# Kernel optimization log

Measured on AMD Instinct MI355X. Metric: run time of the kernel, lower is better.

## Reference

```python
import jax, jax.numpy as jnp
import numpy as np
import math

B, S, D, H = 2, 2048, 1024, 16
DH = D // H  # head_size = 64


def setup_inputs() -> dict:
    key = jax.random.key(0)
    ks = jax.random.split(key, 11)
    s = 0.02
    return {
        "queries": jax.random.normal(ks[0], (B, S, D), jnp.float32),
        "keys": jax.random.normal(ks[1], (B, S, D), jnp.float32),
        "values": jax.random.normal(ks[2], (B, S, D), jnp.float32),
        # nn.Linear weights: y = x @ W.T + b, W has shape (out, in)
        "W_Q": jax.random.normal(ks[3], (D, D), jnp.float32) * s,
        "b_Q": jax.random.normal(ks[4], (D,), jnp.float32) * s,
        "W_K": jax.random.normal(ks[5], (D, D), jnp.float32) * s,
        "b_K": jax.random.normal(ks[6], (D,), jnp.float32) * s,
        "W_V": jax.random.normal(ks[7], (D, D), jnp.float32) * s,
        "b_V": jax.random.normal(ks[8], (D,), jnp.float32) * s,
        "W_O": jax.random.normal(ks[9], (D, D), jnp.float32) * s,
        "b_O": jax.random.normal(ks[10], (D,), jnp.float32) * s,
    }


def _split_heads(x):
    # (B, S, H*DH) -> (B, H, S, DH); torch.chunk+stack == reshape+transpose
    b, s, _ = x.shape
    return x.reshape(b, s, H, DH).transpose(0, 2, 1, 3)


def reference(queries, keys, values, W_Q, b_Q, W_K, b_K, W_V, b_V, W_O, b_O):
    q = _split_heads(queries @ W_Q.T + b_Q)  # (B,H,S,DH)
    k = _split_heads(keys @ W_K.T + b_K)
    v = _split_heads(values @ W_V.T + b_V)

    scale = 1.0 / math.sqrt(DH)
    scores = jnp.einsum("bhqd,bhkd->bhqk", q, k) * scale  # (B,H,S,S)
    causal = jnp.tril(jnp.ones((S, S), dtype=bool))  # allow j <= i (causal)
    scores = jnp.where(causal, scores, -jnp.inf)
    weights = jax.nn.softmax(scores, axis=-1)

    attended = jnp.einsum("bhqk,bhkd->bhqd", weights, v)  # (B,H,S,DH)
    merged = attended.transpose(0, 2, 1, 3).reshape(B, S, D)  # merge_heads
    return merged @ W_O.T + b_O
```

## Files before the change

### kernel.cpp

```cpp
#include <hip/hip_runtime.h>


typedef __bf16 bf16x8 __attribute__((ext_vector_type(8)));
typedef __bf16 bf16x4 __attribute__((ext_vector_type(4)));
typedef float  f32x4  __attribute__((ext_vector_type(4)));
typedef int    i32x2  __attribute__((ext_vector_type(2)));
typedef int    i32x4  __attribute__((ext_vector_type(4)));

#define B_  2
#define S_  2048
#define D_  1024
#define H_  16
#define DH_ 64

#define NEG_ 1.0e30f
#define M2_  5.77078016f
#define QSCALE_ 0.18033688f

#if __has_builtin(__builtin_amdgcn_exp2f)
#define EXP2(x) __builtin_amdgcn_exp2f(x)
#else
#define EXP2(x) __builtin_exp2f(x)
#endif

__device__ __forceinline__ void load_lds16(const __bf16* g, __bf16* lds_base) {
    __builtin_amdgcn_global_load_lds(
        (const __attribute__((address_space(1))) void*)g,
        (__attribute__((address_space(3))) void*)lds_base,
        16, 0, 0);
}

__device__ __forceinline__ int pack_bf16(float lo, float hi) {
    union { int u; __bf16 h[2]; } r;
    r.h[0] = (__bf16)lo; r.h[1] = (__bf16)hi;
    return r.u;
}

__device__ __forceinline__ void p32swap(int& a, int& b, int lane) {
#if __has_builtin(__builtin_amdgcn_permlane32_swap)
    i32x2 r = __builtin_amdgcn_permlane32_swap(a, b, false, false);
    a = r[0]; b = r[1];
#else
    const int addr = ((lane ^ 32) & 63) << 2;
    int ax = __builtin_amdgcn_ds_bpermute(addr, a);
    int bx = __builtin_amdgcn_ds_bpermute(addr, b);
    int na = (lane < 32) ? a : bx;
    int nb = (lane < 32) ? ax : b;
    a = na; b = nb;
#endif
}
__device__ __forceinline__ void p16swap(int& a, int& b, int lane) {
#if __has_builtin(__builtin_amdgcn_permlane16_swap)
    i32x2 r = __builtin_amdgcn_permlane16_swap(a, b, false, false);
    a = r[0]; b = r[1];
#else
    int as = __builtin_amdgcn_ds_swizzle(a, 0x401F);
    int bs = __builtin_amdgcn_ds_swizzle(b, 0x401F);
    const bool odd = (lane >> 4) & 1;
    int na = odd ? bs : a;
    int nb = odd ? b : as;
    a = na; b = nb;
#endif
}

__device__ __forceinline__ bf16x8 cvt8(const float* __restrict__ p) {
    const float4 a = *(const float4*)p;
    const float4 b = *(const float4*)(p + 4);
    bf16x8 r;
    r[0] = (__bf16)a.x; r[1] = (__bf16)a.y; r[2] = (__bf16)a.z; r[3] = (__bf16)a.w;
    r[4] = (__bf16)b.x; r[5] = (__bf16)b.y; r[6] = (__bf16)b.z; r[7] = (__bf16)b.w;
    return r;
}

__global__ void cvt_kernel(const float* __restrict__ q, const float* __restrict__ k,
                           const float* __restrict__ v,
                           const float* __restrict__ wq, const float* __restrict__ wk,
                           const float* __restrict__ wv, const float* __restrict__ wo,
                           __bf16* __restrict__ qb, __bf16* __restrict__ kb,
                           __bf16* __restrict__ vb,
                           __bf16* __restrict__ wqb, __bf16* __restrict__ wkb,
                           __bf16* __restrict__ wvb, __bf16* __restrict__ wob) {
    const int z = blockIdx.z;
    const float* src; __bf16* dst; size_t n;
    switch (z) {
        case 0: src = q;  dst = qb;  n = (size_t)B_ * S_ * D_; break;
        case 1: src = k;  dst = kb;  n = (size_t)B_ * S_ * D_; break;
        case 2: src = v;  dst = vb;  n = (size_t)B_ * S_ * D_; break;
        case 3: src = wq; dst = wqb; n = (size_t)D_ * D_; break;
        case 4: src = wk; dst = wkb; n = (size_t)D_ * D_; break;
        case 5: src = wv; dst = wvb; n = (size_t)D_ * D_; break;
        default: src = wo; dst = wob; n = (size_t)D_ * D_; break;
    }
    const size_t i = ((size_t)blockIdx.x * 256 + threadIdx.x) * 8;
    if (i >= n) return;
    *(bf16x8*)(dst + i) = cvt8(src + i);
}

__device__ __forceinline__ void gemm128_bf(const __bf16* __restrict__ X,
                                           const __bf16* __restrict__ W,
                                           int m0, int n0, int K,
                                           __bf16* As, __bf16* Bs,
                                           f32x4 acc[4][4]) {
    const int tid  = threadIdx.x;
    const int wave = tid >> 6, lane = tid & 63;
    const int row  = lane & 15, quad = lane >> 4;
    const int wm   = wave >> 1, wn = wave & 1;
    const int arow = lane >> 2;
    const int acol = (lane & 3) * 8;

    const f32x4 fzero = {0.f, 0.f, 0.f, 0.f};
#pragma unroll
    for (int mt = 0; mt < 4; ++mt)
#pragma unroll
        for (int nt = 0; nt < 4; ++nt) acc[mt][nt] = fzero;

    auto stage = [&](int buf, int k0) {
#pragma unroll
        for (int c = 0; c < 2; ++c) {
            const int j = wave * 2 + c;
            load_lds16(X + (size_t)(m0 + j * 16 + arow) * K + k0 + acol,
                       As + buf * 4096 + j * 512);
            load_lds16(W + (size_t)(n0 + j * 16 + arow) * K + k0 + acol,
                       Bs + buf * 4096 + j * 512);
        }
    };

    stage(0, 0);
    int cur = 0;
    for (int k0 = 0; k0 < K; k0 += 32) {
        __syncthreads();
        if (k0 + 32 < K) stage(cur ^ 1, k0 + 32);
        const __bf16* Ab = As + cur * 4096;
        const __bf16* Bb = Bs + cur * 4096;
        bf16x8 af[4], bfv[4];
#pragma unroll
        for (int t = 0; t < 4; ++t) {
            af[t]  = *(const bf16x8*)(Ab + (wm * 64 + t * 16 + row) * 32 + quad * 8);
            bfv[t] = *(const bf16x8*)(Bb + (wn * 64 + t * 16 + row) * 32 + quad * 8);
        }
        __builtin_amdgcn_s_setprio(1);
#pragma unroll
        for (int mt = 0; mt < 4; ++mt)
#pragma unroll
            for (int nt = 0; nt < 4; ++nt)
                acc[mt][nt] = __builtin_amdgcn_mfma_f32_16x16x32_bf16(
                    af[mt], bfv[nt], acc[mt][nt], 0, 0, 0);
        __builtin_amdgcn_s_setprio(0);
        cur ^= 1;
    }
}

__global__ void qkv_kernel(const __bf16* __restrict__ qb, const __bf16* __restrict__ kb,
                           const __bf16* __restrict__ vb,
                           const __bf16* __restrict__ wqb, const __bf16* __restrict__ wkb,
                           const __bf16* __restrict__ wvb,
                           const float* __restrict__ bq, const float* __restrict__ bk,
                           const float* __restrict__ bv,
                           __bf16* __restrict__ q_ws, __bf16* __restrict__ k_ws,
                           __bf16* __restrict__ v_ws) {
    __shared__ __align__(16) __bf16 SMEM[16384];
    __bf16* As = SMEM;
    __bf16* Bs = SMEM + 8192;

    const int mode = blockIdx.z;
    const __bf16* X    = mode == 0 ? qb : mode == 1 ? kb : vb;
    const __bf16* W    = mode == 0 ? wqb : mode == 1 ? wkb : wvb;
    const float*  bias = mode == 0 ? bq : mode == 1 ? bk : bv;
    const int m0 = blockIdx.y * 128, n0 = blockIdx.x * 128;

    f32x4 acc[4][4];
    gemm128_bf(X, W, m0, n0, D_, As, Bs, acc);

    const int tid = threadIdx.x;
    const int wave = tid >> 6, lane = tid & 63;
    const int row = lane & 15, quad = lane >> 4;
    const int wm = wave >> 1, wn = wave & 1;

    if (mode == 2) {
        __syncthreads();
        __bf16* T = SMEM;
#pragma unroll
        for (int nt = 0; nt < 4; ++nt) {
            const int nloc = wn * 64 + nt * 16 + row;
            const float bf = bias[n0 + nloc];
#pragma unroll
            for (int mt = 0; mt < 4; ++mt)
#pragma unroll
                for (int r2 = 0; r2 < 4; ++r2) {
                    const int mloc = wm * 64 + mt * 16 + quad * 4 + r2;
                    T[nloc * 128 + ((((mloc >> 3) ^ (nloc & 15)) << 3) | (mloc & 7))] =
                        (__bf16)(acc[mt][nt][r2] + bf);
                }
        }
        __syncthreads();
#pragma unroll
        for (int p = 0; p < 8; ++p) {
            const int nloc = p * 16 + (tid >> 4);
            const int k = tid & 15;
            bf16x8 vv = *(const bf16x8*)(T + nloc * 128 + ((k ^ (nloc & 15)) << 3));
            const int n = n0 + nloc;
            const int h = n >> 6, dh = n & 63;
            const int m = m0 + k * 8;
            const int bb = m >> 11, s = m & (S_ - 1);
            *(bf16x8*)(v_ws + (((size_t)bb * H_ + h) * DH_ + dh) * S_ + s) = vv;
        }
        return;
    }

#pragma unroll
    for (int nt = 0; nt < 4; ++nt) {
        const int n  = n0 + wn * 64 + nt * 16 + row;
        const float bf = bias[n];
        const int h = n >> 6, dh = n & 63;
#pragma unroll
        for (int mt = 0; mt < 4; ++mt) {
#pragma unroll
            for (int r2 = 0; r2 < 4; ++r2) {
                const int m = m0 + wm * 64 + mt * 16 + quad * 4 + r2;
                const int bb = m >> 11, s = m & (S_ - 1);
                const float val = acc[mt][nt][r2] + bf;
                if (mode == 0)
                    q_ws[(((size_t)bb * H_ + h) * S_ + s) * DH_ + dh] = (__bf16)(val * QSCALE_);
                else
                    k_ws[(((size_t)bb * H_ + h) * S_ + s) * DH_ + dh] = (__bf16)val;
            }
        }
    }
}

__global__ __launch_bounds__(256, 4)
void attn_kernel(const __bf16* __restrict__ q_ws, const __bf16* __restrict__ k_ws,
                 const __bf16* __restrict__ v_ws, __bf16* __restrict__ att) {
    __shared__ __align__(16) __bf16 Ks[2 * 64 * 64];
    __shared__ __align__(16) __bf16 Vs[2 * 64 * 64];

    const int id = blockIdx.x;
    const int bh = (id & 7) * 4 + ((id >> 3) & 3);
    const int u = id >> 5, ua = u >> 3, uj = u & 7;
    const int qt = ua * 8 + ((ua & 1) ? (7 - uj) : uj);
    const int tid = threadIdx.x, wave = tid >> 6, lane = tid & 63;
    const int row = lane & 15, quad = lane >> 4;

    const __bf16* Qg = q_ws + ((size_t)bh * S_ + qt * 64 + wave * 16) * DH_;
    const __bf16* Kg = k_ws + (size_t)bh * S_ * DH_;
    const __bf16* Vg = v_ws + (size_t)bh * DH_ * S_;

    bf16x8 qf[2];
#pragma unroll
    for (int ks = 0; ks < 2; ++ks)
        qf[ks] = *(const bf16x8*)(Qg + row * DH_ + ks * 32 + quad * 8);

    bf16x8 onesf;
#pragma unroll
    for (int i = 0; i < 8; ++i) onesf[i] = (__bf16)1.0f;

    const f32x4 fzero = {0.f, 0.f, 0.f, 0.f};
    f32x4 oacc[4];
    f32x4 lacc = fzero;
#pragma unroll
    for (int dt = 0; dt < 4; ++dt) oacc[dt] = fzero;

    const int srow = lane >> 3;
    const int scol = ((lane & 7) ^ srow) * 8;
    const int nkv = qt + 1;

    auto stage = [&](int buf, int kv) {
        __bf16* Kd = Ks + buf * 4096;
        __bf16* Vd = Vs + buf * 4096;
#pragma unroll
        for (int c = 0; c < 2; ++c) {
            const int ck = wave * 2 + c;
            load_lds16(Kg + (size_t)(kv * 64 + ck * 8 + srow) * DH_ + scol, Kd + ck * 512);
            load_lds16(Vg + (size_t)(ck * 8 + srow) * S_ + kv * 64 + scol, Vd + ck * 512);
        }
    };

    stage(0, 0);
    int cur = 0;
    for (int kv = 0; kv < nkv; ++kv) {
        __syncthreads();
        if (kv + 1 < nkv) stage(cur ^ 1, kv + 1);
        const bool diag = (kv == nkv - 1);
        const __bf16* Kb = Ks + cur * 4096;
        const __bf16* Vb = Vs + cur * 4096;
        const int swz = (row & 7) << 3;

#pragma unroll
        for (int kc = 0; kc < 2; ++kc) {
            f32x4 s[2];
            s[0] = fzero; s[1] = fzero;
            __builtin_amdgcn_s_setprio(1);
#pragma unroll
            for (int jn = 0; jn < 2; ++jn) {
                const int nt = kc * 2 + jn;
                const int kb = (nt * 16 + row) * 64 + quad * 8;
                bf16x8 kf0 = *(const bf16x8*)(Kb + (kb ^ swz));
                bf16x8 kf1 = *(const bf16x8*)(Kb + ((kb + 32) ^ swz));
                s[jn] = __builtin_amdgcn_mfma_f32_16x16x32_bf16(kf0, qf[0], s[jn], 0, 0, 0);
                s[jn] = __builtin_amdgcn_mfma_f32_16x16x32_bf16(kf1, qf[1], s[jn], 0, 0, 0);
            }
            __builtin_amdgcn_s_setprio(0);

            if (diag) {
                const int rloc = wave * 16 + row;
#pragma unroll
                for (int jn = 0; jn < 2; ++jn)
#pragma unroll
                    for (int r = 0; r < 4; ++r) {
                        const int cloc = kc * 32 + jn * 16 + quad * 4 + r;
                        if (cloc > rloc) s[jn][r] = -NEG_;
                    }
            }

            float p0[4], p1[4];
#pragma unroll
            for (int r = 0; r < 4; ++r) {
                p0[r] = EXP2(s[0][r] - M2_);
                p1[r] = EXP2(s[1][r] - M2_);
            }
            int a0 = pack_bf16(p0[0], p0[1]), a1 = pack_bf16(p0[2], p0[3]);
            int b0 = pack_bf16(p1[0], p1[1]), b1 = pack_bf16(p1[2], p1[3]);
            p32swap(a0, b0, lane); p16swap(a0, b0, lane);
            p32swap(a1, b1, lane); p16swap(a1, b1, lane);
            union { i32x4 i; bf16x8 v; } pu;
            pu.i = (i32x4){a0, a1, b0, b1};
            const bf16x8 pf = pu.v;

            __builtin_amdgcn_s_setprio(1);
#pragma unroll
            for (int dt = 0; dt < 4; ++dt) {
                const int vb = (dt * 16 + row) * 64 + kc * 32 + quad * 8;
                bf16x8 vf = *(const bf16x8*)(Vb + (vb ^ swz));
                oacc[dt] = __builtin_amdgcn_mfma_f32_16x16x32_bf16(vf, pf, oacc[dt], 0, 0, 0);
            }
            lacc = __builtin_amdgcn_mfma_f32_16x16x32_bf16(onesf, pf, lacc, 0, 0, 0);
            __builtin_amdgcn_s_setprio(0);
        }
        cur ^= 1;
    }

    const int b = bh >> 4, h = bh & 15;
    const float inv = 1.f / lacc[0];
    const int srow2 = qt * 64 + wave * 16 + row;
    __bf16* obase = att + ((size_t)b * S_ + srow2) * D_ + h * DH_;
#pragma unroll
    for (int dt = 0; dt < 4; ++dt) {
        bf16x4 o;
#pragma unroll
        for (int r = 0; r < 4; ++r) o[r] = (__bf16)(oacc[dt][r] * inv);
        *(bf16x4*)(obase + dt * 16 + quad * 4) = o;
    }
}

__global__ void oproj_kernel(const __bf16* __restrict__ attn, const __bf16* __restrict__ wob,
                             const float* __restrict__ bo, float* __restrict__ out) {
    __shared__ __align__(16) __bf16 SMEM[16384];
    __bf16* As = SMEM;
    __bf16* Bs = SMEM + 8192;
    const int m0 = blockIdx.y * 128, n0 = blockIdx.x * 128;

    f32x4 acc[4][4];
    gemm128_bf(attn, wob, m0, n0, D_, As, Bs, acc);

    const int tid = threadIdx.x;
    const int wave = tid >> 6, lane = tid & 63;
    const int row = lane & 15, quad = lane >> 4;
    const int wm = wave >> 1, wn = wave & 1;

#pragma unroll
    for (int nt = 0; nt < 4; ++nt) {
        const int n = n0 + wn * 64 + nt * 16 + row;
        const float bf = bo[n];
#pragma unroll
        for (int mt = 0; mt < 4; ++mt) {
#pragma unroll
            for (int r = 0; r < 4; ++r) {
                const int m = m0 + wm * 64 + mt * 16 + quad * 4 + r;
                out[(size_t)m * D_ + n] = acc[mt][nt][r] + bf;
            }
        }
    }
}

extern "C" void kernel_launch(void* const* d_in, const int* in_sizes, int n_in,
                              void* d_out, int out_size, void* d_ws, size_t ws_size,
                              hipStream_t stream) {
    const float* q_in = (const float*)d_in[0];
    const float* k_in = (const float*)d_in[1];
    const float* v_in = (const float*)d_in[2];
    const float* wq   = (const float*)d_in[3];
    const float* bq   = (const float*)d_in[4];
    const float* wk   = (const float*)d_in[5];
    const float* bk   = (const float*)d_in[6];
    const float* wv   = (const float*)d_in[7];
    const float* bv   = (const float*)d_in[8];
    const float* wo   = (const float*)d_in[9];
    const float* bo   = (const float*)d_in[10];

    char* ws = (char*)d_ws;
    const size_t MB = 1024 * 1024;
    __bf16* qb   = (__bf16*)(ws);
    __bf16* kb   = (__bf16*)(ws + 8 * MB);
    __bf16* vb   = (__bf16*)(ws + 16 * MB);
    __bf16* wqb  = (__bf16*)(ws + 24 * MB);
    __bf16* wkb  = (__bf16*)(ws + 26 * MB);
    __bf16* wvb  = (__bf16*)(ws + 28 * MB);
    __bf16* wob  = (__bf16*)(ws + 30 * MB);
    __bf16* q_ws = (__bf16*)(ws + 32 * MB);
    __bf16* k_ws = (__bf16*)(ws + 40 * MB);
    __bf16* v_ws = (__bf16*)(ws + 48 * MB);
    __bf16* attb = qb;
    float*  out  = (float*)d_out;

    cvt_kernel<<<dim3(2048, 1, 7), 256, 0, stream>>>(
        q_in, k_in, v_in, wq, wk, wv, wo, qb, kb, vb, wqb, wkb, wvb, wob);
    qkv_kernel<<<dim3(D_ / 128, (B_ * S_) / 128, 3), 256, 0, stream>>>(
        qb, kb, vb, wqb, wkb, wvb, bq, bk, bv, q_ws, k_ws, v_ws);
    attn_kernel<<<dim3(32 * 32), 256, 0, stream>>>(q_ws, k_ws, v_ws, attb);
    oproj_kernel<<<dim3(D_ / 128, (B_ * S_) / 128), 256, 0, stream>>>(attb, wob, bo, out);
}
```

Measured before the change: 209.2 us.

## Pair complementary causal query tiles per attention block to share K/V loads

Each attention block now handles two query tiles, j and 31-j, so every block does the same amount of causal work. K/V tiles staged in LDS, and the K fragments read from them, are reused by both tiles, which halves the grid to 512 blocks. Launch bounds drop to 2 blocks per SM to leave room for the doubled accumulators and Q fragments. In exchange, register pressure rises, occupancy may fall, and the branches on act1 add control flow.

```diff
diff --git a/kernel.cpp b/kernel.cpp
--- a/kernel.cpp
+++ b/kernel.cpp
@@ -228,7 +228,7 @@
     }
 }
 
-__global__ __launch_bounds__(256, 4)
+__global__ __launch_bounds__(256, 2)
 void attn_kernel(const __bf16* __restrict__ q_ws, const __bf16* __restrict__ k_ws,
                  const __bf16* __restrict__ v_ws, __bf16* __restrict__ att) {
     __shared__ __align__(16) __bf16 Ks[2 * 64 * 64];
@@ -236,33 +236,42 @@
 
     const int id = blockIdx.x;
     const int bh = (id & 7) * 4 + ((id >> 3) & 3);
-    const int u = id >> 5, ua = u >> 3, uj = u & 7;
-    const int qt = ua * 8 + ((ua & 1) ? (7 - uj) : uj);
+    const int u = (id >> 5) & 7;
+    const int j = (id >> 8) ? (15 - u) : u;
+    const int qt0 = 31 - j, qt1 = j;
     const int tid = threadIdx.x, wave = tid >> 6, lane = tid & 63;
     const int row = lane & 15, quad = lane >> 4;
 
-    const __bf16* Qg = q_ws + ((size_t)bh * S_ + qt * 64 + wave * 16) * DH_;
     const __bf16* Kg = k_ws + (size_t)bh * S_ * DH_;
     const __bf16* Vg = v_ws + (size_t)bh * DH_ * S_;
 
-    bf16x8 qf[2];
-#pragma unroll
-    for (int ks = 0; ks < 2; ++ks)
-        qf[ks] = *(const bf16x8*)(Qg + row * DH_ + ks * 32 + quad * 8);
+    bf16x8 qf[2][2];
+#pragma unroll
+    for (int st = 0; st < 2; ++st) {
+        const int qts = st ? qt1 : qt0;
+        const __bf16* Qg = q_ws + ((size_t)bh * S_ + qts * 64 + wave * 16) * DH_;
+#pragma unroll
+        for (int ks = 0; ks < 2; ++ks)
+            qf[st][ks] = *(const bf16x8*)(Qg + row * DH_ + ks * 32 + quad * 8);
+    }
 
     bf16x8 onesf;
 #pragma unroll
     for (int i = 0; i < 8; ++i) onesf[i] = (__bf16)1.0f;
 
     const f32x4 fzero = {0.f, 0.f, 0.f, 0.f};
-    f32x4 oacc[4];
-    f32x4 lacc = fzero;
-#pragma unroll
-    for (int dt = 0; dt < 4; ++dt) oacc[dt] = fzero;
+    f32x4 oacc[2][4];
+    f32x4 lacc[2];
+#pragma unroll
+    for (int st = 0; st < 2; ++st) {
+        lacc[st] = fzero;
+#pragma unroll
+        for (int dt = 0; dt < 4; ++dt) oacc[st][dt] = fzero;
+    }
 
     const int srow = lane >> 3;
     const int scol = ((lane & 7) ^ srow) * 8;
-    const int nkv = qt + 1;
+    const int nkv = qt0 + 1;
 
     auto stage = [&](int buf, int kv) {
         __bf16* Kd = Ks + buf * 4096;
@@ -280,75 +289,113 @@
     for (int kv = 0; kv < nkv; ++kv) {
         __syncthreads();
         if (kv + 1 < nkv) stage(cur ^ 1, kv + 1);
-        const bool diag = (kv == nkv - 1);
         const __bf16* Kb = Ks + cur * 4096;
         const __bf16* Vb = Vs + cur * 4096;
+        const bool act1 = (kv <= qt1);
         const int swz = (row & 7) << 3;
 
 #pragma unroll
         for (int kc = 0; kc < 2; ++kc) {
-            f32x4 s[2];
-            s[0] = fzero; s[1] = fzero;
+            bf16x8 kf[2][2];
+#pragma unroll
+            for (int jn = 0; jn < 2; ++jn) {
+                const int kb = ((kc * 2 + jn) * 16 + row) * 64 + quad * 8;
+                kf[jn][0] = *(const bf16x8*)(Kb + (kb ^ swz));
+                kf[jn][1] = *(const bf16x8*)(Kb + ((kb + 32) ^ swz));
+            }
+            f32x4 s[2][2];
             __builtin_amdgcn_s_setprio(1);
 #pragma unroll
             for (int jn = 0; jn < 2; ++jn) {
-                const int nt = kc * 2 + jn;
-                const int kb = (nt * 16 + row) * 64 + quad * 8;
-                bf16x8 kf0 = *(const bf16x8*)(Kb + (kb ^ swz));
-                bf16x8 kf1 = *(const bf16x8*)(Kb + ((kb + 32) ^ swz));
-                s[jn] = __builtin_amdgcn_mfma_f32_16x16x32_bf16(kf0, qf[0], s[jn], 0, 0, 0);
-                s[jn] = __builtin_amdgcn_mfma_f32_16x16x32_bf16(kf1, qf[1], s[jn], 0, 0, 0);
+                s[0][jn] = fzero;
+                s[0][jn] = __builtin_amdgcn_mfma_f32_16x16x32_bf16(kf[jn][0], qf[0][0], s[0][jn], 0, 0, 0);
+                s[0][jn] = __builtin_amdgcn_mfma_f32_16x16x32_bf16(kf[jn][1], qf[0][1], s[0][jn], 0, 0, 0);
+            }
+            if (act1) {
+#pragma unroll
+                for (int jn = 0; jn < 2; ++jn) {
+                    s[1][jn] = fzero;
+                    s[1][jn] = __builtin_amdgcn_mfma_f32_16x16x32_bf16(kf[jn][0], qf[1][0], s[1][jn], 0, 0, 0);
+                    s[1][jn] = __builtin_amdgcn_mfma_f32_16x16x32_bf16(kf[jn][1], qf[1][1], s[1][jn], 0, 0, 0);
+                }
             }
             __builtin_amdgcn_s_setprio(0);
 
-            if (diag) {
-                const int rloc = wave * 16 + row;
+            const int rloc = wave * 16 + row;
+            if (kv == qt0) {
 #pragma unroll
                 for (int jn = 0; jn < 2; ++jn)
 #pragma unroll
                     for (int r = 0; r < 4; ++r) {
                         const int cloc = kc * 32 + jn * 16 + quad * 4 + r;
-                        if (cloc > rloc) s[jn][r] = -NEG_;
+                        if (cloc > rloc) s[0][jn][r] = -NEG_;
                     }
             }
-
-            float p0[4], p1[4];
-#pragma unroll
-            for (int r = 0; r < 4; ++r) {
-                p0[r] = EXP2(s[0][r] - M2_);
-                p1[r] = EXP2(s[1][r] - M2_);
-            }
-            int a0 = pack_bf16(p0[0], p0[1]), a1 = pack_bf16(p0[2], p0[3]);
-            int b0 = pack_bf16(p1[0], p1[1]), b1 = pack_bf16(p1[2], p1[3]);
-            p32swap(a0, b0, lane); p16swap(a0, b0, lane);
-            p32swap(a1, b1, lane); p16swap(a1, b1, lane);
-            union { i32x4 i; bf16x8 v; } pu;
-            pu.i = (i32x4){a0, a1, b0, b1};
-            const bf16x8 pf = pu.v;
+            if (act1 && kv == qt1) {
+#pragma unroll
+                for (int jn = 0; jn < 2; ++jn)
+#pragma unroll
+                    for (int r = 0; r < 4; ++r) {
+                        const int cloc = kc * 32 + jn * 16 + quad * 4 + r;
+                        if (cloc > rloc) s[1][jn][r] = -NEG_;
+                    }
+            }
+
+            bf16x8 pf[2];
+            {
+                int a0 = pack_bf16(EXP2(s[0][0][0] - M2_), EXP2(s[0][0][1] - M2_));
+                int a1 = pack_bf16(EXP2(s[0][0][2] - M2_), EXP2(s[0][0][3] - M2_));
+                int b0 = pack_bf16(EXP2(s[0][1][0] - M2_), EXP2(s[0][1][1] - M2_));
+                int b1 = pack_bf16(EXP2(s[0][1][2] - M2_), EXP2(s[0][1][3] - M2_));
+                p32swap(a0, b0, lane); p16swap(a0, b0, lane);
+                p32swap(a1, b1, lane); p16swap(a1, b1, lane);
+                union { i32x4 i; bf16x8 v; } pu;
+                pu.i = (i32x4){a0, a1, b0, b1};
+                pf[0] = pu.v;
+            }
+            if (act1) {
+                int a0 = pack_bf16(EXP2(s[1][0][0] - M2_), EXP2(s[1][0][1] - M2_));
+                int a1 = pack_bf16(EXP2(s[1][0][2] - M2_), EXP2(s[1][0][3] - M2_));
+                int b0 = pack_bf16(EXP2(s[1][1][0] - M2_), EXP2(s[1][1][1] - M2_));
+                int b1 = pack_bf16(EXP2(s[1][1][2] - M2_), EXP2(s[1][1][3] - M2_));
+                p32swap(a0, b0, lane); p16swap(a0, b0, lane);
+                p32swap(a1, b1, lane); p16swap(a1, b1, lane);
+                union { i32x4 i; bf16x8 v; } pu;
+                pu.i = (i32x4){a0, a1, b0, b1};
+                pf[1] = pu.v;
+            }
 
             __builtin_amdgcn_s_setprio(1);
 #pragma unroll
             for (int dt = 0; dt < 4; ++dt) {
                 const int vb = (dt * 16 + row) * 64 + kc * 32 + quad * 8;
                 bf16x8 vf = *(const bf16x8*)(Vb + (vb ^ swz));
-                oacc[dt] = __builtin_amdgcn_mfma_f32_16x16x32_bf16(vf, pf, oacc[dt], 0, 0, 0);
-            }
-            lacc = __builtin_amdgcn_mfma_f32_16x16x32_bf16(onesf, pf, lacc, 0, 0, 0);
+                oacc[0][dt] = __builtin_amdgcn_mfma_f32_16x16x32_bf16(vf, pf[0], oacc[0][dt], 0, 0, 0);
+                if (act1)
+                    oacc[1][dt] = __builtin_amdgcn_mfma_f32_16x16x32_bf16(vf, pf[1], oacc[1][dt], 0, 0, 0);
+            }
+            lacc[0] = __builtin_amdgcn_mfma_f32_16x16x32_bf16(onesf, pf[0], lacc[0], 0, 0, 0);
+            if (act1)
+                lacc[1] = __builtin_amdgcn_mfma_f32_16x16x32_bf16(onesf, pf[1], lacc[1], 0, 0, 0);
             __builtin_amdgcn_s_setprio(0);
         }
         cur ^= 1;
     }
 
     const int b = bh >> 4, h = bh & 15;
-    const float inv = 1.f / lacc[0];
-    const int srow2 = qt * 64 + wave * 16 + row;
-    __bf16* obase = att + ((size_t)b * S_ + srow2) * D_ + h * DH_;
-#pragma unroll
-    for (int dt = 0; dt < 4; ++dt) {
-        bf16x4 o;
-#pragma unroll
-        for (int r = 0; r < 4; ++r) o[r] = (__bf16)(oacc[dt][r] * inv);
-        *(bf16x4*)(obase + dt * 16 + quad * 4) = o;
+#pragma unroll
+    for (int st = 0; st < 2; ++st) {
+        const int qts = st ? qt1 : qt0;
+        const float inv = 1.f / lacc[st][0];
+        const int srow2 = qts * 64 + wave * 16 + row;
+        __bf16* obase = att + ((size_t)b * S_ + srow2) * D_ + h * DH_;
+#pragma unroll
+        for (int dt = 0; dt < 4; ++dt) {
+            bf16x4 o;
+#pragma unroll
+            for (int r = 0; r < 4; ++r) o[r] = (__bf16)(oacc[st][dt][r] * inv);
+            *(bf16x4*)(obase + dt * 16 + quad * 4) = o;
+        }
     }
 }
 
@@ -416,6 +463,6 @@
         q_in, k_in, v_in, wq, wk, wv, wo, qb, kb, vb, wqb, wkb, wvb, wob);
     qkv_kernel<<<dim3(D_ / 128, (B_ * S_) / 128, 3), 256, 0, stream>>>(
         qb, kb, vb, wqb, wkb, wvb, bq, bk, bv, q_ws, k_ws, v_ws);
-    attn_kernel<<<dim3(32 * 32), 256, 0, stream>>>(q_ws, k_ws, v_ws, attb);
+    attn_kernel<<<dim3(512), 256, 0, stream>>>(q_ws, k_ws, v_ws, attb);
     oproj_kernel<<<dim3(D_ / 128, (B_ * S_) / 128), 256, 0, stream>>>(attb, wob, bo, out);
 }
```

Result: slower. 216.0 us (+3.3%).

## Fuse fp32-to-bf16 conversion into GEMM tile loads, drop separate convert kernel

Applied to the files above, without the earlier changes.

Removes the standalone conversion kernel. The QKV and output-projection GEMMs now read fp32 inputs and weights straight from global memory into registers, convert them to bf16, and write them into LDS after the MFMA block, so the register-staged loads are software-pipelined. The bf16 attention output still goes through the async global-to-LDS path. This removes a full extra read and write pass over the activations and weights, at the cost of fp32 global loads inside the GEMM, extra registers, and losing the direct-to-LDS load path for fp32 operands. Each weight tile is now converted again by every block that uses it.

```diff
diff --git a/kernel.cpp b/kernel.cpp
--- a/kernel.cpp
+++ b/kernel.cpp
@@ -34,6 +34,13 @@
     union { int u; __bf16 h[2]; } r;
     r.h[0] = (__bf16)lo; r.h[1] = (__bf16)hi;
     return r.u;
+}
+
+__device__ __forceinline__ bf16x8 cvt44(const float4 a, const float4 b) {
+    bf16x8 r;
+    r[0] = (__bf16)a.x; r[1] = (__bf16)a.y; r[2] = (__bf16)a.z; r[3] = (__bf16)a.w;
+    r[4] = (__bf16)b.x; r[5] = (__bf16)b.y; r[6] = (__bf16)b.z; r[7] = (__bf16)b.w;
+    return r;
 }
 
 __device__ __forceinline__ void p32swap(int& a, int& b, int lane) {
@@ -63,44 +70,13 @@
 #endif
 }
 
-__device__ __forceinline__ bf16x8 cvt8(const float* __restrict__ p) {
-    const float4 a = *(const float4*)p;
-    const float4 b = *(const float4*)(p + 4);
-    bf16x8 r;
-    r[0] = (__bf16)a.x; r[1] = (__bf16)a.y; r[2] = (__bf16)a.z; r[3] = (__bf16)a.w;
-    r[4] = (__bf16)b.x; r[5] = (__bf16)b.y; r[6] = (__bf16)b.z; r[7] = (__bf16)b.w;
-    return r;
-}
-
-__global__ void cvt_kernel(const float* __restrict__ q, const float* __restrict__ k,
-                           const float* __restrict__ v,
-                           const float* __restrict__ wq, const float* __restrict__ wk,
-                           const float* __restrict__ wv, const float* __restrict__ wo,
-                           __bf16* __restrict__ qb, __bf16* __restrict__ kb,
-                           __bf16* __restrict__ vb,
-                           __bf16* __restrict__ wqb, __bf16* __restrict__ wkb,
-                           __bf16* __restrict__ wvb, __bf16* __restrict__ wob) {
-    const int z = blockIdx.z;
-    const float* src; __bf16* dst; size_t n;
-    switch (z) {
-        case 0: src = q;  dst = qb;  n = (size_t)B_ * S_ * D_; break;
-        case 1: src = k;  dst = kb;  n = (size_t)B_ * S_ * D_; break;
-        case 2: src = v;  dst = vb;  n = (size_t)B_ * S_ * D_; break;
-        case 3: src = wq; dst = wqb; n = (size_t)D_ * D_; break;
-        case 4: src = wk; dst = wkb; n = (size_t)D_ * D_; break;
-        case 5: src = wv; dst = wvb; n = (size_t)D_ * D_; break;
-        default: src = wo; dst = wob; n = (size_t)D_ * D_; break;
-    }
-    const size_t i = ((size_t)blockIdx.x * 256 + threadIdx.x) * 8;
-    if (i >= n) return;
-    *(bf16x8*)(dst + i) = cvt8(src + i);
-}
-
-__device__ __forceinline__ void gemm128_bf(const __bf16* __restrict__ X,
-                                           const __bf16* __restrict__ W,
-                                           int m0, int n0, int K,
-                                           __bf16* As, __bf16* Bs,
-                                           f32x4 acc[4][4]) {
+template<bool A_BF16>
+__device__ __forceinline__ void gemm128_f(const float* __restrict__ Xf,
+                                          const __bf16* __restrict__ Xh,
+                                          const float* __restrict__ W,
+                                          int m0, int n0, int K,
+                                          __bf16* As, __bf16* Bs,
+                                          f32x4 acc[4][4]) {
     const int tid  = threadIdx.x;
     const int wave = tid >> 6, lane = tid & 63;
     const int row  = lane & 15, quad = lane >> 4;
@@ -114,22 +90,54 @@
 #pragma unroll
         for (int nt = 0; nt < 4; ++nt) acc[mt][nt] = fzero;
 
-    auto stage = [&](int buf, int k0) {
+    float4 ra[2][2], rb[2][2];
+
+    auto loadA = [&](int k0) {
 #pragma unroll
         for (int c = 0; c < 2; ++c) {
-            const int j = wave * 2 + c;
-            load_lds16(X + (size_t)(m0 + j * 16 + arow) * K + k0 + acol,
-                       As + buf * 4096 + j * 512);
-            load_lds16(W + (size_t)(n0 + j * 16 + arow) * K + k0 + acol,
-                       Bs + buf * 4096 + j * 512);
-        }
-    };
-
-    stage(0, 0);
+            const float* p = Xf + (size_t)(m0 + (wave * 2 + c) * 16 + arow) * K + k0 + acol;
+            ra[c][0] = *(const float4*)p;
+            ra[c][1] = *(const float4*)(p + 4);
+        }
+    };
+    auto writeA = [&](int buf) {
+#pragma unroll
+        for (int c = 0; c < 2; ++c)
+            *(bf16x8*)(As + buf * 4096 + (wave * 2 + c) * 512 + lane * 8) =
+                cvt44(ra[c][0], ra[c][1]);
+    };
+    auto stageA = [&](int buf, int k0) {
+#pragma unroll
+        for (int c = 0; c < 2; ++c)
+            load_lds16(Xh + (size_t)(m0 + (wave * 2 + c) * 16 + arow) * K + k0 + acol,
+                       As + buf * 4096 + (wave * 2 + c) * 512);
+    };
+    auto loadB = [&](int k0) {
+#pragma unroll
+        for (int c = 0; c < 2; ++c) {
+            const float* p = W + (size_t)(n0 + (wave * 2 + c) * 16 + arow) * K + k0 + acol;
+            rb[c][0] = *(const float4*)p;
+            rb[c][1] = *(const float4*)(p + 4);
+        }
+    };
+    auto writeB = [&](int buf) {
+#pragma unroll
+        for (int c = 0; c < 2; ++c)
+            *(bf16x8*)(Bs + buf * 4096 + (wave * 2 + c) * 512 + lane * 8) =
+                cvt44(rb[c][0], rb[c][1]);
+    };
+
+    if (A_BF16) stageA(0, 0); else { loadA(0); writeA(0); }
+    loadB(0); writeB(0);
+
     int cur = 0;
     for (int k0 = 0; k0 < K; k0 += 32) {
         __syncthreads();
-        if (k0 + 32 < K) stage(cur ^ 1, k0 + 32);
+        const bool more = (k0 + 32 < K);
+        if (more) {
+            if (A_BF16) stageA(cur ^ 1, k0 + 32); else loadA(k0 + 32);
+            loadB(k0 + 32);
+        }
         const __bf16* Ab = As + cur * 4096;
         const __bf16* Bb = Bs + cur * 4096;
         bf16x8 af[4], bfv[4];
@@ -146,14 +154,18 @@
                 acc[mt][nt] = __builtin_amdgcn_mfma_f32_16x16x32_bf16(
                     af[mt], bfv[nt], acc[mt][nt], 0, 0, 0);
         __builtin_amdgcn_s_setprio(0);
+        if (more) {
+            if (!A_BF16) writeA(cur ^ 1);
+            writeB(cur ^ 1);
+        }
         cur ^= 1;
     }
 }
 
-__global__ void qkv_kernel(const __bf16* __restrict__ qb, const __bf16* __restrict__ kb,
-                           const __bf16* __restrict__ vb,
-                           const __bf16* __restrict__ wqb, const __bf16* __restrict__ wkb,
-                           const __bf16* __restrict__ wvb,
+__global__ void qkv_kernel(const float* __restrict__ q, const float* __restrict__ k,
+                           const float* __restrict__ v,
+                           const float* __restrict__ wq, const float* __restrict__ wk,
+                           const float* __restrict__ wv,
                            const float* __restrict__ bq, const float* __restrict__ bk,
                            const float* __restrict__ bv,
                            __bf16* __restrict__ q_ws, __bf16* __restrict__ k_ws,
@@ -163,13 +175,13 @@
     __bf16* Bs = SMEM + 8192;
 
     const int mode = blockIdx.z;
-    const __bf16* X    = mode == 0 ? qb : mode == 1 ? kb : vb;
-    const __bf16* W    = mode == 0 ? wqb : mode == 1 ? wkb : wvb;
-    const float*  bias = mode == 0 ? bq : mode == 1 ? bk : bv;
+    const float* X    = mode == 0 ? q : mode == 1 ? k : v;
+    const float* W    = mode == 0 ? wq : mode == 1 ? wk : wv;
+    const float* bias = mode == 0 ? bq : mode == 1 ? bk : bv;
     const int m0 = blockIdx.y * 128, n0 = blockIdx.x * 128;
 
     f32x4 acc[4][4];
-    gemm128_bf(X, W, m0, n0, D_, As, Bs, acc);
+    gemm128_f<false>(X, nullptr, W, m0, n0, D_, As, Bs, acc);
 
     const int tid = threadIdx.x;
     const int wave = tid >> 6, lane = tid & 63;
@@ -196,11 +208,11 @@
 #pragma unroll
         for (int p = 0; p < 8; ++p) {
             const int nloc = p * 16 + (tid >> 4);
-            const int k = tid & 15;
-            bf16x8 vv = *(const bf16x8*)(T + nloc * 128 + ((k ^ (nloc & 15)) << 3));
+            const int kk = tid & 15;
+            bf16x8 vv = *(const bf16x8*)(T + nloc * 128 + ((kk ^ (nloc & 15)) << 3));
             const int n = n0 + nloc;
             const int h = n >> 6, dh = n & 63;
-            const int m = m0 + k * 8;
+            const int m = m0 + kk * 8;
             const int bb = m >> 11, s = m & (S_ - 1);
             *(bf16x8*)(v_ws + (((size_t)bb * H_ + h) * DH_ + dh) * S_ + s) = vv;
         }
@@ -352,7 +364,7 @@
     }
 }
 
-__global__ void oproj_kernel(const __bf16* __restrict__ attn, const __bf16* __restrict__ wob,
+__global__ void oproj_kernel(const __bf16* __restrict__ attn, const float* __restrict__ wo,
                              const float* __restrict__ bo, float* __restrict__ out) {
     __shared__ __align__(16) __bf16 SMEM[16384];
     __bf16* As = SMEM;
@@ -360,7 +372,7 @@
     const int m0 = blockIdx.y * 128, n0 = blockIdx.x * 128;
 
     f32x4 acc[4][4];
-    gemm128_bf(attn, wob, m0, n0, D_, As, Bs, acc);
+    gemm128_f<true>(nullptr, attn, wo, m0, n0, D_, As, Bs, acc);
 
     const int tid = threadIdx.x;
     const int wave = tid >> 6, lane = tid & 63;
@@ -399,23 +411,14 @@
 
     char* ws = (char*)d_ws;
     const size_t MB = 1024 * 1024;
-    __bf16* qb   = (__bf16*)(ws);
-    __bf16* kb   = (__bf16*)(ws + 8 * MB);
-    __bf16* vb   = (__bf16*)(ws + 16 * MB);
-    __bf16* wqb  = (__bf16*)(ws + 24 * MB);
-    __bf16* wkb  = (__bf16*)(ws + 26 * MB);
-    __bf16* wvb  = (__bf16*)(ws + 28 * MB);
-    __bf16* wob  = (__bf16*)(ws + 30 * MB);
-    __bf16* q_ws = (__bf16*)(ws + 32 * MB);
-    __bf16* k_ws = (__bf16*)(ws + 40 * MB);
-    __bf16* v_ws = (__bf16*)(ws + 48 * MB);
-    __bf16* attb = qb;
+    __bf16* attb = (__bf16*)(ws);
+    __bf16* q_ws = (__bf16*)(ws + 8 * MB);
+    __bf16* k_ws = (__bf16*)(ws + 16 * MB);
+    __bf16* v_ws = (__bf16*)(ws + 24 * MB);
     float*  out  = (float*)d_out;
 
-    cvt_kernel<<<dim3(2048, 1, 7), 256, 0, stream>>>(
-        q_in, k_in, v_in, wq, wk, wv, wo, qb, kb, vb, wqb, wkb, wvb, wob);
     qkv_kernel<<<dim3(D_ / 128, (B_ * S_) / 128, 3), 256, 0, stream>>>(
-        qb, kb, vb, wqb, wkb, wvb, bq, bk, bv, q_ws, k_ws, v_ws);
+        q_in, k_in, v_in, wq, wk, wv, bq, bk, bv, q_ws, k_ws, v_ws);
     attn_kernel<<<dim3(32 * 32), 256, 0, stream>>>(q_ws, k_ws, v_ws, attb);
-    oproj_kernel<<<dim3(D_ / 128, (B_ * S_) / 128), 256, 0, stream>>>(attb, wob, bo, out);
-}
+    oproj_kernel<<<dim3(D_ / 128, (B_ * S_) / 128), 256, 0, stream>>>(attb, wo, bo, out);
+}
```

Result: slower. 363.2 us (+73.6%).
